# Optimization experiments

Hardware: AMD Instinct MI355X
Metric: run time of the kernel (lower is better)

## Reference

```python
import jax, jax.numpy as jnp
import numpy as np

N = 4096        # nodes
E = 131072      # edges (avg degree 32)
IN_F = 256      # in_features
OUT_F = 64      # out_features per head
H = 8           # num_heads


def setup_inputs() -> dict:
    key = jax.random.key(0)
    k1, k2, k3, k4 = jax.random.split(key, 4)
    x = jax.random.normal(k1, (N, IN_F), dtype=jnp.float32)
    # xavier-ish scales for the learned params
    W = jax.random.normal(k2, (IN_F, OUT_F * H), dtype=jnp.float32) * 0.06
    a = jax.random.normal(k3, (2 * OUT_F, 1), dtype=jnp.float32) * 0.12
    edge_index = jax.random.randint(k4, (2, E), 0, N, dtype=jnp.int32)
    return {"x": x, "W": W, "a": a, "edge_index": edge_index}


def reference(x, W, a, edge_index):
    n = x.shape[0]
    Wh = (x @ W).reshape(n, H, OUT_F)          # [N, H, F]
    src, dst = edge_index[0], edge_index[1]
    # edge score: cat(Wh[src], Wh[dst]) @ a == Wh[src]@a1 + Wh[dst]@a2
    a1 = a[:OUT_F, 0]                           # [F]
    a2 = a[OUT_F:2 * OUT_F, 0]                  # [F]
    alpha_src = Wh @ a1                         # [N, H]
    alpha_dst = Wh @ a2                         # [N, H]
    edge_e = jax.nn.leaky_relu(alpha_src[src] + alpha_dst[dst], 0.2)  # [E, H]
    # dense scatter exactly as the original module (non-edges stay 0 in softmax)
    attention = jnp.zeros((n, n, H), dtype=x.dtype).at[src, dst].set(edge_e)
    attention = jax.nn.softmax(attention, axis=1)
    # dropout is identity in eval mode
    h_prime = jnp.einsum('nmh,mhf->nhf', attention, Wh)  # [N, H, F]
    return h_prime.reshape(n, H * OUT_F)        # concat=True
```

## Files before the change

### kernel.cpp

```cpp
#include <hip/hip_runtime.h>
#include <hip/hip_bf16.h>

constexpr int NN    = 4096;
constexpr int EE    = 131072;
constexpr int IN_F  = 256;
constexpr int OUT_F = 64;
constexpr int HH    = 8;
constexpr int HF    = OUT_F * HH;
constexpr int CAP   = 128;

__device__ __forceinline__ unsigned short f2b(float f) {
    unsigned int u = __float_as_uint(f);
    u = u + 0x7FFFu + ((u >> 16) & 1u);
    return (unsigned short)(u >> 16);
}
__device__ __forceinline__ float b2f(unsigned int lo16) {
    return __uint_as_float(lo16 << 16);
}

#define TM 64
#define TN 64
#define TK 32

__global__ __launch_bounds__(256) void gemm_fused(const float* __restrict__ x,
                                                  const float* __restrict__ W,
                                                  const float* __restrict__ a,
                                                  unsigned short* __restrict__ Whb,
                                                  float* __restrict__ asrc,
                                                  float* __restrict__ adst,
                                                  float* __restrict__ S) {
    __shared__ float As[TK][TM + 4];
    __shared__ float Bs[TK][TN + 4];
    __shared__ float Scol[TN];
    int t  = threadIdx.x;
    int tx = t & 15;
    int ty = t >> 4;
    int m0 = blockIdx.x * TM;
    int n0 = blockIdx.y * TN;
    float acc[4][4] = {};

    float4 pa[2], pb[2];
    {
        int k0 = 0;
#pragma unroll
        for (int i = 0; i < 2; ++i) {
            int flat = i * 256 + t, row = flat >> 3, c4 = flat & 7;
            pa[i] = *(const float4*)(x + (size_t)(m0 + row) * IN_F + k0 + c4 * 4);
        }
#pragma unroll
        for (int i = 0; i < 2; ++i) {
            int flat = i * 256 + t, row = flat >> 4, c4 = flat & 15;
            pb[i] = *(const float4*)(W + (size_t)(k0 + row) * HF + n0 + c4 * 4);
        }
    }

    for (int k0 = 0; k0 < IN_F; k0 += TK) {
#pragma unroll
        for (int i = 0; i < 2; ++i) {
            int flat = i * 256 + t, row = flat >> 3, c4 = flat & 7;
            As[c4 * 4 + 0][row] = pa[i].x;
            As[c4 * 4 + 1][row] = pa[i].y;
            As[c4 * 4 + 2][row] = pa[i].z;
            As[c4 * 4 + 3][row] = pa[i].w;
        }
#pragma unroll
        for (int i = 0; i < 2; ++i) {
            int flat = i * 256 + t, row = flat >> 4, c4 = flat & 15;
            *(float4*)(&Bs[row][c4 * 4]) = pb[i];
        }
        __syncthreads();
        if (k0 + TK < IN_F) {
            int kn = k0 + TK;
#pragma unroll
            for (int i = 0; i < 2; ++i) {
                int flat = i * 256 + t, row = flat >> 3, c4 = flat & 7;
                pa[i] = *(const float4*)(x + (size_t)(m0 + row) * IN_F + kn + c4 * 4);
            }
#pragma unroll
            for (int i = 0; i < 2; ++i) {
                int flat = i * 256 + t, row = flat >> 4, c4 = flat & 15;
                pb[i] = *(const float4*)(W + (size_t)(kn + row) * HF + n0 + c4 * 4);
            }
        }
#pragma unroll
        for (int k = 0; k < TK; ++k) {
            float4 a4 = *(const float4*)(&As[k][ty * 4]);
            float4 b4 = *(const float4*)(&Bs[k][tx * 4]);
            float av[4] = {a4.x, a4.y, a4.z, a4.w};
            float bv[4] = {b4.x, b4.y, b4.z, b4.w};
#pragma unroll
            for (int ii = 0; ii < 4; ++ii)
#pragma unroll
                for (int jj = 0; jj < 4; ++jj)
                    acc[ii][jj] += av[ii] * bv[jj];
        }
        __syncthreads();
    }

#pragma unroll
    for (int ii = 0; ii < 4; ++ii) {
        ushort4 v;
        v.x = f2b(acc[ii][0]);
        v.y = f2b(acc[ii][1]);
        v.z = f2b(acc[ii][2]);
        v.w = f2b(acc[ii][3]);
        *(ushort4*)(Whb + (size_t)(m0 + ty * 4 + ii) * HF + n0 + tx * 4) = v;
    }

    int h = n0 >> 6;
    float a1v[4], a2v[4];
#pragma unroll
    for (int jj = 0; jj < 4; ++jj) {
        int f = tx * 4 + jj;
        a1v[jj] = a[f];
        a2v[jj] = a[OUT_F + f];
    }
#pragma unroll
    for (int ii = 0; ii < 4; ++ii) {
        float p1 = 0.f, p2 = 0.f;
#pragma unroll
        for (int jj = 0; jj < 4; ++jj) {
            p1 += acc[ii][jj] * a1v[jj];
            p2 += acc[ii][jj] * a2v[jj];
        }
#pragma unroll
        for (int mask = 1; mask < 16; mask <<= 1) {
            p1 += __shfl_xor(p1, mask);
            p2 += __shfl_xor(p2, mask);
        }
        if (tx == 0) {
            int node = m0 + ty * 4 + ii;
            asrc[node * HH + h] = p1;
            adst[node * HH + h] = p2;
        }
    }

    if (t < TN) Scol[t] = 0.f;
    __syncthreads();
#pragma unroll
    for (int jj = 0; jj < 4; ++jj) {
        float cs = acc[0][jj] + acc[1][jj] + acc[2][jj] + acc[3][jj];
        atomicAdd(&Scol[tx * 4 + jj], cs);
    }
    __syncthreads();
    if (t < TN) atomicAdd(&S[n0 + t], Scol[t]);
}

__global__ __launch_bounds__(256) void scatter_edges(const int* __restrict__ src,
                                                     const int* __restrict__ dst,
                                                     const float* __restrict__ asrc,
                                                     const float* __restrict__ adst,
                                                     unsigned int* __restrict__ bitmap,
                                                     int* __restrict__ cnt,
                                                     int* __restrict__ csr_dst,
                                                     float* __restrict__ csr_w) {
    int e = blockIdx.x * 256 + threadIdx.x;
    if (e >= EE) return;
    int s = src[e], d = dst[e];
    unsigned int bitidx = ((unsigned int)s << 12) | (unsigned int)d;
    unsigned int word   = bitidx >> 5;
    unsigned int mask   = 1u << (bitidx & 31);
    unsigned int old    = atomicOr(&bitmap[word], mask);
    if (!(old & mask)) {
        int pos  = atomicAdd(&cnt[s], 1);
        int slot = (s << 7) + pos;
        csr_dst[slot] = d;
        float4 s0 = *(const float4*)(asrc + s * HH);
        float4 s1 = *(const float4*)(asrc + s * HH + 4);
        float4 d0 = *(const float4*)(adst + d * HH);
        float4 d1 = *(const float4*)(adst + d * HH + 4);
        float ev[8] = {s0.x + d0.x, s0.y + d0.y, s0.z + d0.z, s0.w + d0.w,
                       s1.x + d1.x, s1.y + d1.y, s1.z + d1.z, s1.w + d1.w};
        float w[8];
#pragma unroll
        for (int h = 0; h < 8; ++h) {
            float x = ev[h];
            x = (x > 0.f) ? x : 0.2f * x;
            w[h] = __expf(x) - 1.f;
        }
        float4 w0 = {w[0], w[1], w[2], w[3]};
        float4 w1 = {w[4], w[5], w[6], w[7]};
        *(float4*)(csr_w + (size_t)slot * 8)     = w0;
        *(float4*)(csr_w + (size_t)slot * 8 + 4) = w1;
    }
}

__global__ __launch_bounds__(512) void aggregate_kernel(const unsigned short* __restrict__ Whb,
                                                        const float* __restrict__ S,
                                                        const int* __restrict__ cnt,
                                                        const int* __restrict__ csr_dst,
                                                        const float* __restrict__ csr_w,
                                                        float* __restrict__ out) {
    __shared__ float wbuf[CAP * HH];
    __shared__ int   midx[CAP];
    __shared__ float red[4][HF];
    __shared__ float denom[HH];
    int i = blockIdx.x;
    int t = threadIdx.x;
    int deg = cnt[i];

    const float* wrow = csr_w + ((size_t)i << 7) * HH;
    for (int idx = t; idx < deg * HH; idx += 512) wbuf[idx] = wrow[idx];
    if (t < deg) midx[t] = csr_dst[(i << 7) + t];
    __syncthreads();

    if (t < 128) {
        int h = t >> 4, ln = t & 15;
        float p = 0.f;
        for (int sl = ln; sl < deg; sl += 16) p += wbuf[sl * HH + h];
#pragma unroll
        for (int mask = 1; mask < 16; mask <<= 1) p += __shfl_xor(p, mask);
        if (ln == 0) denom[h] = (float)NN + p;
    }
    __syncthreads();

    int g = t >> 7;
    int r = t & 127;
    int h = r >> 4;
    float4 acc = {0.f, 0.f, 0.f, 0.f};

    int j = g;
    int   mC = 0; float wC = 0.f; uint2 uC = {0u, 0u};
    if (j < deg) {
        mC = midx[j];
        wC = wbuf[j * HH + h];
        uC = *(const uint2*)(Whb + ((size_t)mC << 9) + (r << 2));
    }
    while (j < deg) {
        int jn = j + 4;
        int   mN = 0; float wN = 0.f; uint2 uN = {0u, 0u};
        if (jn < deg) {
            mN = midx[jn];
            wN = wbuf[jn * HH + h];
            uN = *(const uint2*)(Whb + ((size_t)mN << 9) + (r << 2));
        }
        float v0 = b2f(uC.x & 0xFFFFu);
        float v1 = b2f(uC.x >> 16);
        float v2 = b2f(uC.y & 0xFFFFu);
        float v3 = b2f(uC.y >> 16);
        acc.x += wC * v0;
        acc.y += wC * v1;
        acc.z += wC * v2;
        acc.w += wC * v3;
        mC = mN; wC = wN; uC = uN;
        j = jn;
    }

    *(float4*)(&red[g][r << 2]) = acc;
    __syncthreads();

    float tot = red[0][t] + red[1][t] + red[2][t] + red[3][t] + S[t];
    out[((size_t)i << 9) + t] = tot / denom[t >> 6];
}

extern "C" void kernel_launch(void* const* d_in, const int* in_sizes, int n_in,
                              void* d_out, int out_size, void* d_ws, size_t ws_size,
                              hipStream_t stream) {
    const float* x  = (const float*)d_in[0];
    const float* W  = (const float*)d_in[1];
    const float* a  = (const float*)d_in[2];
    const int*   ei = (const int*)d_in[3];
    const int* src = ei;
    const int* dst = ei + EE;
    float* out = (float*)d_out;

    char* ws = (char*)d_ws;
    unsigned short* Whb = (unsigned short*)(ws + 0);
    float* asrc     = (float*)(ws + 4194304);
    float* adst     = (float*)(ws + 4325376);
    int*   csr_dst  = (int*)  (ws + 4456448);
    float* csr_w    = (float*)(ws + 6553600);
    float* S        = (float*)(ws + 23330816);
    int*   cnt      = (int*)  (ws + 23332864);
    unsigned int* bitmap = (unsigned int*)(ws + 23349248);

    hipMemsetAsync(ws + 23330816, 0, 2048 + 16384 + 2097152, stream);

    gemm_fused<<<dim3(NN / TM, HF / TN), 256, 0, stream>>>(x, W, a, Whb, asrc, adst, S);

    scatter_edges<<<EE / 256, 256, 0, stream>>>(src, dst, asrc, adst, bitmap, cnt,
                                                csr_dst, csr_w);

    aggregate_kernel<<<NN, 512, 0, stream>>>(Whb, S, cnt, csr_dst, csr_w, out);
}
```

Measured before the change: 130.8 us.

## Move edge weight computation and dedup into aggregate, slim scatter to CSR build

The scatter kernel no longer uses a 2MB dedup bitmap or computes per-edge attention weights. It only appends destinations to per-source CSR slots, so it can run before the GEMM. The aggregate kernel now finds duplicate edges with an O(deg^2) scan in shared memory and computes the leaky-relu/exp weights itself from asrc/adst. This removes the bitmap memset and the csr_w global round trip. Aggregation also moves to 8 groups with 16-byte loads of 8 bf16 values per thread, at the cost of a quadratic duplicate check and a capped degree.

```diff
diff --git a/kernel.cpp b/kernel.cpp
--- a/kernel.cpp
+++ b/kernel.cpp
@@ -41,16 +41,15 @@
 
     float4 pa[2], pb[2];
     {
-        int k0 = 0;
 #pragma unroll
         for (int i = 0; i < 2; ++i) {
             int flat = i * 256 + t, row = flat >> 3, c4 = flat & 7;
-            pa[i] = *(const float4*)(x + (size_t)(m0 + row) * IN_F + k0 + c4 * 4);
+            pa[i] = *(const float4*)(x + (size_t)(m0 + row) * IN_F + c4 * 4);
         }
 #pragma unroll
         for (int i = 0; i < 2; ++i) {
             int flat = i * 256 + t, row = flat >> 4, c4 = flat & 15;
-            pb[i] = *(const float4*)(W + (size_t)(k0 + row) * HF + n0 + c4 * 4);
+            pb[i] = *(const float4*)(W + (size_t)row * HF + n0 + c4 * 4);
         }
     }
 
@@ -146,62 +145,58 @@
     if (t < TN) atomicAdd(&S[n0 + t], Scol[t]);
 }
 
-__global__ __launch_bounds__(256) void scatter_edges(const int* __restrict__ src,
-                                                     const int* __restrict__ dst,
-                                                     const float* __restrict__ asrc,
-                                                     const float* __restrict__ adst,
-                                                     unsigned int* __restrict__ bitmap,
-                                                     int* __restrict__ cnt,
-                                                     int* __restrict__ csr_dst,
-                                                     float* __restrict__ csr_w) {
+__global__ __launch_bounds__(256) void scatter_lite(const int* __restrict__ src,
+                                                    const int* __restrict__ dst,
+                                                    int* __restrict__ cnt,
+                                                    int* __restrict__ csr_dst) {
     int e = blockIdx.x * 256 + threadIdx.x;
     if (e >= EE) return;
     int s = src[e], d = dst[e];
-    unsigned int bitidx = ((unsigned int)s << 12) | (unsigned int)d;
-    unsigned int word   = bitidx >> 5;
-    unsigned int mask   = 1u << (bitidx & 31);
-    unsigned int old    = atomicOr(&bitmap[word], mask);
-    if (!(old & mask)) {
-        int pos  = atomicAdd(&cnt[s], 1);
-        int slot = (s << 7) + pos;
-        csr_dst[slot] = d;
-        float4 s0 = *(const float4*)(asrc + s * HH);
-        float4 s1 = *(const float4*)(asrc + s * HH + 4);
-        float4 d0 = *(const float4*)(adst + d * HH);
-        float4 d1 = *(const float4*)(adst + d * HH + 4);
-        float ev[8] = {s0.x + d0.x, s0.y + d0.y, s0.z + d0.z, s0.w + d0.w,
-                       s1.x + d1.x, s1.y + d1.y, s1.z + d1.z, s1.w + d1.w};
-        float w[8];
-#pragma unroll
-        for (int h = 0; h < 8; ++h) {
-            float x = ev[h];
-            x = (x > 0.f) ? x : 0.2f * x;
-            w[h] = __expf(x) - 1.f;
-        }
-        float4 w0 = {w[0], w[1], w[2], w[3]};
-        float4 w1 = {w[4], w[5], w[6], w[7]};
-        *(float4*)(csr_w + (size_t)slot * 8)     = w0;
-        *(float4*)(csr_w + (size_t)slot * 8 + 4) = w1;
-    }
+    int pos = atomicAdd(&cnt[s], 1);
+    csr_dst[(s << 7) + pos] = d;
 }
 
 __global__ __launch_bounds__(512) void aggregate_kernel(const unsigned short* __restrict__ Whb,
+                                                        const float* __restrict__ asrc,
+                                                        const float* __restrict__ adst,
                                                         const float* __restrict__ S,
                                                         const int* __restrict__ cnt,
                                                         const int* __restrict__ csr_dst,
-                                                        const float* __restrict__ csr_w,
                                                         float* __restrict__ out) {
-    __shared__ float wbuf[CAP * HH];
-    __shared__ int   midx[CAP];
-    __shared__ float red[4][HF];
-    __shared__ float denom[HH];
+    __shared__ int           midx[CAP];
+    __shared__ unsigned char dupf[CAP];
+    __shared__ float         wbuf[CAP * HH];
+    __shared__ float         as_sh[HH];
+    __shared__ float         denom[HH];
+    __shared__ float         red[8][HF];
     int i = blockIdx.x;
     int t = threadIdx.x;
     int deg = cnt[i];
-
-    const float* wrow = csr_w + ((size_t)i << 7) * HH;
-    for (int idx = t; idx < deg * HH; idx += 512) wbuf[idx] = wrow[idx];
-    if (t < deg) midx[t] = csr_dst[(i << 7) + t];
+    if (deg > CAP) deg = CAP;
+
+    if (t < HH) as_sh[t] = asrc[i * HH + t];
+    for (int j = t; j < deg; j += 512) midx[j] = csr_dst[(i << 7) + j];
+    __syncthreads();
+
+    for (int j = t; j < deg; j += 512) {
+        int m = midx[j];
+        unsigned char f = 0;
+        for (int k = 0; k < j; ++k)
+            if (midx[k] == m) { f = 1; break; }
+        dupf[j] = f;
+    }
+    __syncthreads();
+
+    for (int idx = t; idx < deg * HH; idx += 512) {
+        int sl = idx >> 3, h = idx & 7;
+        float w = 0.f;
+        if (!dupf[sl]) {
+            float xv = as_sh[h] + adst[midx[sl] * HH + h];
+            xv = (xv > 0.f) ? xv : 0.2f * xv;
+            w = __expf(xv) - 1.f;
+        }
+        wbuf[idx] = w;
+    }
     __syncthreads();
 
     if (t < 128) {
@@ -214,42 +209,46 @@
     }
     __syncthreads();
 
-    int g = t >> 7;
-    int r = t & 127;
-    int h = r >> 4;
-    float4 acc = {0.f, 0.f, 0.f, 0.f};
+    int g = t >> 6;
+    int r = t & 63;
+    int h = r >> 3;
+    float accv[8] = {};
 
     int j = g;
-    int   mC = 0; float wC = 0.f; uint2 uC = {0u, 0u};
+    uint4 uC = {0, 0, 0, 0};
+    float wC = 0.f;
     if (j < deg) {
-        mC = midx[j];
         wC = wbuf[j * HH + h];
-        uC = *(const uint2*)(Whb + ((size_t)mC << 9) + (r << 2));
+        uC = *(const uint4*)(Whb + ((size_t)midx[j] << 9) + (r << 3));
     }
     while (j < deg) {
-        int jn = j + 4;
-        int   mN = 0; float wN = 0.f; uint2 uN = {0u, 0u};
+        int jn = j + 8;
+        uint4 uN = {0, 0, 0, 0};
+        float wN = 0.f;
         if (jn < deg) {
-            mN = midx[jn];
             wN = wbuf[jn * HH + h];
-            uN = *(const uint2*)(Whb + ((size_t)mN << 9) + (r << 2));
-        }
-        float v0 = b2f(uC.x & 0xFFFFu);
-        float v1 = b2f(uC.x >> 16);
-        float v2 = b2f(uC.y & 0xFFFFu);
-        float v3 = b2f(uC.y >> 16);
-        acc.x += wC * v0;
-        acc.y += wC * v1;
-        acc.z += wC * v2;
-        acc.w += wC * v3;
-        mC = mN; wC = wN; uC = uN;
-        j = jn;
-    }
-
-    *(float4*)(&red[g][r << 2]) = acc;
-    __syncthreads();
-
-    float tot = red[0][t] + red[1][t] + red[2][t] + red[3][t] + S[t];
+            uN = *(const uint4*)(Whb + ((size_t)midx[jn] << 9) + (r << 3));
+        }
+        accv[0] += wC * b2f(uC.x & 0xFFFFu);
+        accv[1] += wC * b2f(uC.x >> 16);
+        accv[2] += wC * b2f(uC.y & 0xFFFFu);
+        accv[3] += wC * b2f(uC.y >> 16);
+        accv[4] += wC * b2f(uC.z & 0xFFFFu);
+        accv[5] += wC * b2f(uC.z >> 16);
+        accv[6] += wC * b2f(uC.w & 0xFFFFu);
+        accv[7] += wC * b2f(uC.w >> 16);
+        uC = uN; wC = wN; j = jn;
+    }
+
+    float4 v0 = {accv[0], accv[1], accv[2], accv[3]};
+    float4 v1 = {accv[4], accv[5], accv[6], accv[7]};
+    *(float4*)(&red[g][r * 8])     = v0;
+    *(float4*)(&red[g][r * 8 + 4]) = v1;
+    __syncthreads();
+
+    float tot = S[t];
+#pragma unroll
+    for (int gg = 0; gg < 8; ++gg) tot += red[gg][t];
     out[((size_t)i << 9) + t] = tot / denom[t >> 6];
 }
 
@@ -269,17 +268,14 @@
     float* asrc     = (float*)(ws + 4194304);
     float* adst     = (float*)(ws + 4325376);
     int*   csr_dst  = (int*)  (ws + 4456448);
-    float* csr_w    = (float*)(ws + 6553600);
-    float* S        = (float*)(ws + 23330816);
-    int*   cnt      = (int*)  (ws + 23332864);
-    unsigned int* bitmap = (unsigned int*)(ws + 23349248);
-
-    hipMemsetAsync(ws + 23330816, 0, 2048 + 16384 + 2097152, stream);
+    float* S        = (float*)(ws + 6553600);
+    int*   cnt      = (int*)  (ws + 6555648);
+
+    hipMemsetAsync(ws + 6553600, 0, 2048 + 16384, stream);
+
+    scatter_lite<<<EE / 256, 256, 0, stream>>>(src, dst, cnt, csr_dst);
 
     gemm_fused<<<dim3(NN / TM, HF / TN), 256, 0, stream>>>(x, W, a, Whb, asrc, adst, S);
 
-    scatter_edges<<<EE / 256, 256, 0, stream>>>(src, dst, asrc, adst, bitmap, cnt,
-                                                csr_dst, csr_w);
-
-    aggregate_kernel<<<NN, 512, 0, stream>>>(Whb, S, cnt, csr_dst, csr_w, out);
-}
+    aggregate_kernel<<<NN, 512, 0, stream>>>(Whb, asrc, adst, S, cnt, csr_dst, out);
+}
```

Result: no change. 132.3 us (+1.1%).
